# Performance work log

Measured on AMD Instinct MI355X. Metric: run time of the kernel, lower is better.

## Reference

```python
import jax, jax.numpy as jnp
import numpy as np

B, IN, H, O, L, G = 4096, 512, 1024, 256, 2, 3


def _lin_init(key, out_dim, in_dim):
    k1, k2 = jax.random.split(key)
    bound = 1.0 / np.sqrt(in_dim)
    w = jax.random.uniform(k1, (out_dim, in_dim), jnp.float32, -bound, bound)
    b = jax.random.uniform(k2, (out_dim,), jnp.float32, -bound, bound)
    return w, b


def setup_inputs() -> dict:
    key = jax.random.key(0)
    ks = jax.random.split(key, 10)
    x = jax.random.normal(ks[0], (B, IN), jnp.float32)
    hidden = jax.random.normal(ks[1], (L, B, H), jnp.float32)
    i2d_w, i2d_b = _lin_init(ks[2], H, IN)
    # stacked GRU params, PyTorch gate order (r, z, n); layer0 input dim == H (after i2d)
    kih = jax.random.split(ks[3], L)
    khh = jax.random.split(ks[4], L)
    gru_w_ih = jnp.stack([_lin_init(kih[l], 3 * H, H)[0] for l in range(L)])
    gru_b_ih = jnp.stack([_lin_init(kih[l], 3 * H, H)[1] for l in range(L)])
    gru_w_hh = jnp.stack([_lin_init(khh[l], 3 * H, H)[0] for l in range(L)])
    gru_b_hh = jnp.stack([_lin_init(khh[l], 3 * H, H)[1] for l in range(L)])
    mu_w, mu_b = _lin_init(ks[5], O * G, H)
    sigma_w, sigma_b = _lin_init(ks[6], O * G, H)
    pi_w, pi_b = _lin_init(ks[7], O * G, H)
    return {"x": x, "hidden": hidden, "i2d_w": i2d_w, "i2d_b": i2d_b,
            "gru_w_ih": gru_w_ih, "gru_w_hh": gru_w_hh,
            "gru_b_ih": gru_b_ih, "gru_b_hh": gru_b_hh,
            "mu_w": mu_w, "mu_b": mu_b, "sigma_w": sigma_w, "sigma_b": sigma_b,
            "pi_w": pi_w, "pi_b": pi_b, "batch_size": B}


def reference(x, hidden, i2d_w, i2d_b, gru_w_ih, gru_w_hh, gru_b_ih, gru_b_hh,
              mu_w, mu_b, sigma_w, sigma_b, pi_w, pi_b, batch_size):
    # input projection + relu
    h1 = jax.nn.relu(x @ i2d_w.T + i2d_b)  # [B, H]
    # single-timestep stacked GRU (PyTorch cell math, gate order r,z,n)
    inp = h1
    new_h = []
    for l in range(hidden.shape[0]):
        h_prev = hidden[l]
        gi = inp @ gru_w_ih[l].T + gru_b_ih[l]   # [B, 3H]
        gh = h_prev @ gru_w_hh[l].T + gru_b_hh[l]
        i_r, i_z, i_n = jnp.split(gi, 3, axis=-1)
        h_r, h_z, h_n = jnp.split(gh, 3, axis=-1)
        r = jax.nn.sigmoid(i_r + h_r)
        z = jax.nn.sigmoid(i_z + h_z)
        n = jnp.tanh(i_n + r * h_n)
        h_new = (1.0 - z) * n + z * h_prev
        new_h.append(h_new)
        inp = h_new
    hidden_out = jnp.stack(new_h)            # [L, B, H]
    h_out = jnp.tanh(inp)                    # [B, H]
    n_g = 3
    o = mu_w.shape[0] // n_g
    pi = jax.nn.softmax((h_out @ pi_w.T + pi_b).reshape(-1, n_g, o), axis=1)
    mu = (h_out @ mu_w.T + mu_b).reshape(-1, n_g, o)
    sig = jax.nn.softplus(h_out @ sigma_w.T + sigma_b).reshape(-1, n_g, o)
    return (mu, sig, pi, hidden_out)
```

## Files before the change

kernel.cpp:

```cpp
#include <hip/hip_runtime.h>
#include <stdint.h>

typedef unsigned short bf16u;
typedef float f32x4 __attribute__((ext_vector_type(4)));
typedef short bf16x8 __attribute__((ext_vector_type(8)));
typedef float f4 __attribute__((ext_vector_type(4)));

#define BM 128
#define BN 128
#define BK 64

__device__ __forceinline__ float b2f(bf16u u) {
  union { uint32_t i; float f; } v; v.i = ((uint32_t)u) << 16; return v.f;
}
__device__ __forceinline__ uint32_t f2b(float f) {
  union { float f; uint32_t i; } v; v.f = f;
  uint32_t i = v.i;
  return (i + 0x7FFFu + ((i >> 16) & 1u)) >> 16;
}
__device__ __forceinline__ float sigm(float x) { return 1.f / (1.f + __expf(-x)); }

__global__ __launch_bounds__(256)
void cvt_f32_bf16(const float* __restrict__ src, bf16u* __restrict__ dst) {
  size_t i = ((size_t)blockIdx.x * 256 + threadIdx.x) * 8;
  f4 a = *(const f4*)&src[i];
  f4 b = *(const f4*)&src[i + 4];
  uint4 o;
  o.x = (f2b(a[0]) & 0xffffu) | (f2b(a[1]) << 16);
  o.y = (f2b(a[2]) & 0xffffu) | (f2b(a[3]) << 16);
  o.z = (f2b(b[0]) & 0xffffu) | (f2b(b[1]) << 16);
  o.w = (f2b(b[2]) & 0xffffu) | (f2b(b[3]) << 16);
  *(uint4*)&dst[i] = o;
}

struct GemmPtrs {
  const bf16u* A[3];
  const bf16u* W[3];
  const float* bias[3];
  void* C[3];
};

template <int ACT, int OUTF32>
__global__ __launch_bounds__(256)
void gemm_bt(GemmPtrs p, int N, int K) {
  __shared__ bf16u sA[BM * BK];
  __shared__ bf16u sB[BN * BK];
  const int z = blockIdx.z;
  const bf16u* __restrict__ A = p.A[z];
  const bf16u* __restrict__ W = p.W[z];
  const float* __restrict__ bias = p.bias[z];

  const int tid  = threadIdx.x;
  const int wave = tid >> 6;
  const int lane = tid & 63;
  const int bn = blockIdx.x, bm = blockIdx.y;

  const int srow = wave * 32 + (lane >> 3);
  const int kc   = (lane & 7) ^ ((lane >> 3) & 7);
  const bf16u* ag = A + (size_t)(bm * BM + srow) * K + kc * 8;
  const bf16u* wg = W + (size_t)(bn * BN + srow) * K + kc * 8;

  const int wm = wave >> 1, wn = wave & 1;
  const int q = lane >> 4, cl = lane & 15;

  int aoff[4][2], boff[4][2];
#pragma unroll
  for (int i = 0; i < 4; ++i) {
    int m = wm * 64 + i * 16 + cl;
    int n = wn * 64 + i * 16 + cl;
#pragma unroll
    for (int kk = 0; kk < 2; ++kk) {
      aoff[i][kk] = m * 64 + (((q + kk * 4) ^ (m & 7)) * 8);
      boff[i][kk] = n * 64 + (((q + kk * 4) ^ (n & 7)) * 8);
    }
  }

  f32x4 acc[4][4] = {};

  for (int k0 = 0; k0 < K; k0 += BK) {
#pragma unroll
    for (int t = 0; t < 4; ++t) {
      __builtin_amdgcn_global_load_lds(
          (const __attribute__((address_space(1))) void*)(ag + k0 + (size_t)t * 8 * K),
          (__attribute__((address_space(3))) void*)&sA[wave * 2048 + t * 512],
          16, 0, 0);
      __builtin_amdgcn_global_load_lds(
          (const __attribute__((address_space(1))) void*)(wg + k0 + (size_t)t * 8 * K),
          (__attribute__((address_space(3))) void*)&sB[wave * 2048 + t * 512],
          16, 0, 0);
    }
    __syncthreads();
#pragma unroll
    for (int kk = 0; kk < 2; ++kk) {
      bf16x8 af[4], bfr[4];
#pragma unroll
      for (int i = 0; i < 4; ++i) af[i] = *(const bf16x8*)&sA[aoff[i][kk]];
#pragma unroll
      for (int j = 0; j < 4; ++j) bfr[j] = *(const bf16x8*)&sB[boff[j][kk]];
#pragma unroll
      for (int i = 0; i < 4; ++i)
#pragma unroll
        for (int j = 0; j < 4; ++j)
          acc[i][j] = __builtin_amdgcn_mfma_f32_16x16x32_bf16(af[i], bfr[j], acc[i][j], 0, 0, 0);
    }
    __syncthreads();
  }

  float bv[4];
#pragma unroll
  for (int j = 0; j < 4; ++j)
    bv[j] = bias[bn * BN + wn * 64 + j * 16 + cl];

  const int row0 = bm * BM + wm * 64 + q * 4;
  const int col0 = bn * BN + wn * 64 + cl;
#pragma unroll
  for (int i = 0; i < 4; ++i)
#pragma unroll
    for (int j = 0; j < 4; ++j)
#pragma unroll
      for (int r = 0; r < 4; ++r) {
        float v = acc[i][j][r] + bv[j];
        if (ACT == 1) v = fmaxf(v, 0.f);
        size_t off = (size_t)(row0 + i * 16 + r) * N + (col0 + j * 16);
        if (OUTF32) ((float*)p.C[z])[off] = v;
        else        ((bf16u*)p.C[z])[off] = (bf16u)f2b(v);
      }
}

struct __align__(16) V8 { uint32_t u[4]; };
__device__ __forceinline__ float getf(const V8& v, int k) {
  uint32_t w = v.u[k >> 1];
  return b2f((bf16u)((k & 1) ? (w >> 16) : (w & 0xffffu)));
}
__device__ __forceinline__ void setb(V8& v, int k, float f) {
  uint32_t b = f2b(f) & 0xffffu;
  if (k & 1) v.u[k >> 1] = (v.u[k >> 1] & 0x0000ffffu) | (b << 16);
  else       v.u[k >> 1] = (v.u[k >> 1] & 0xffff0000u) | b;
}

template <int LAST>
__global__ __launch_bounds__(256)
void gru_gates(const bf16u* __restrict__ gi, const bf16u* __restrict__ gh,
               const float* __restrict__ hprev, float* __restrict__ hid_out,
               bf16u* __restrict__ nxt) {
  int t = blockIdx.x * 256 + threadIdx.x;
  size_t idx = (size_t)t * 8;
  int b = (int)(idx >> 10);
  int h = (int)(idx & 1023);
  size_t g0 = (size_t)b * 3072 + h;
  V8 ir  = *(const V8*)&gi[g0];
  V8 izv = *(const V8*)&gi[g0 + 1024];
  V8 inv = *(const V8*)&gi[g0 + 2048];
  V8 hr  = *(const V8*)&gh[g0];
  V8 hzv = *(const V8*)&gh[g0 + 1024];
  V8 hnv = *(const V8*)&gh[g0 + 2048];
  f4 hp0 = *(const f4*)&hprev[idx];
  f4 hp1 = *(const f4*)&hprev[idx + 4];
  f4 o0, o1;
  V8 no = {};
#pragma unroll
  for (int k = 0; k < 8; ++k) {
    float hpv = (k < 4) ? hp0[k] : hp1[k - 4];
    float r  = sigm(getf(ir, k) + getf(hr, k));
    float zg = sigm(getf(izv, k) + getf(hzv, k));
    float n  = tanhf(getf(inv, k) + r * getf(hnv, k));
    float hnew = (1.f - zg) * n + zg * hpv;
    if (k < 4) o0[k] = hnew; else o1[k - 4] = hnew;
    setb(no, k, LAST ? tanhf(hnew) : hnew);
  }
  *(f4*)&hid_out[idx] = o0;
  *(f4*)&hid_out[idx + 4] = o1;
  *(V8*)&nxt[idx] = no;
}

__global__ __launch_bounds__(256)
void heads_ep(const float* __restrict__ raw, float* __restrict__ out,
              int rawHS, int outHS) {
  int t = blockIdx.x * 256 + threadIdx.x;
  int b = t >> 6;
  int o4 = (t & 63) << 2;
  size_t rb = (size_t)b * 768 + o4;
  f4 mu[3], sg[3], pi[3];
#pragma unroll
  for (int g = 0; g < 3; ++g) {
    mu[g] = *(const f4*)&raw[rb + g * 256];
    sg[g] = *(const f4*)&raw[(size_t)rawHS + rb + g * 256];
    pi[g] = *(const f4*)&raw[2 * (size_t)rawHS + rb + g * 256];
  }
  f4 pe[3];
#pragma unroll
  for (int c = 0; c < 4; ++c) {
    float m = fmaxf(fmaxf(pi[0][c], pi[1][c]), pi[2][c]);
    float e0 = __expf(pi[0][c] - m), e1 = __expf(pi[1][c] - m), e2 = __expf(pi[2][c] - m);
    float s = 1.f / (e0 + e1 + e2);
    pe[0][c] = e0 * s; pe[1][c] = e1 * s; pe[2][c] = e2 * s;
  }
#pragma unroll
  for (int g = 0; g < 3; ++g) {
    f4 sp;
#pragma unroll
    for (int c = 0; c < 4; ++c)
      sp[c] = fmaxf(sg[g][c], 0.f) + log1pf(__expf(-fabsf(sg[g][c])));
    *(f4*)&out[rb + g * 256]                     = mu[g];
    *(f4*)&out[(size_t)outHS + rb + g * 256]     = sp;
    *(f4*)&out[2 * (size_t)outHS + rb + g * 256] = pe[g];
  }
}

extern "C" void kernel_launch(void* const* d_in, const int* in_sizes, int n_in,
                              void* d_out, int out_size, void* d_ws, size_t ws_size,
                              hipStream_t stream) {
  const float* x      = (const float*)d_in[0];
  const float* hidden = (const float*)d_in[1];
  const float* i2d_w  = (const float*)d_in[2];
  const float* i2d_b  = (const float*)d_in[3];
  const float* w_ih   = (const float*)d_in[4];
  const float* w_hh   = (const float*)d_in[5];
  const float* b_ih   = (const float*)d_in[6];
  const float* b_hh   = (const float*)d_in[7];
  const float* mu_w   = (const float*)d_in[8];
  const float* mu_b   = (const float*)d_in[9];
  const float* sg_w   = (const float*)d_in[10];
  const float* sg_b   = (const float*)d_in[11];
  const float* pi_w   = (const float*)d_in[12];
  const float* pi_b   = (const float*)d_in[13];
  float* out = (float*)d_out;

  const size_t BH = 4194304;
  const int HS = 3145728;
  float* hid_base = out + (size_t)3 * HS;

  dim3 blk(256, 1, 1);

  bf16u* wb = (bf16u*)d_ws;
  bf16u* wb_i2d = wb;
  bf16u* wb_ih  = wb_i2d + 524288;
  bf16u* wb_hh  = wb_ih + 6291456;
  bf16u* wb_mu  = wb_hh + 6291456;
  bf16u* wb_sg  = wb_mu + 786432;
  bf16u* wb_pi  = wb_sg + 786432;
  const size_t wbytes = 30932992;

  cvt_f32_bf16<<<dim3(524288 / 2048), blk, 0, stream>>>(i2d_w, wb_i2d);
  cvt_f32_bf16<<<dim3(6291456 / 2048), blk, 0, stream>>>(w_ih, wb_ih);
  cvt_f32_bf16<<<dim3(6291456 / 2048), blk, 0, stream>>>(w_hh, wb_hh);
  cvt_f32_bf16<<<dim3(786432 / 2048), blk, 0, stream>>>(mu_w, wb_mu);
  cvt_f32_bf16<<<dim3(786432 / 2048), blk, 0, stream>>>(sg_w, wb_sg);
  cvt_f32_bf16<<<dim3(786432 / 2048), blk, 0, stream>>>(pi_w, wb_pi);

  int Bc = 4096;
  while (wbytes + (size_t)Bc * 19456 > ws_size && Bc > 256) Bc >>= 1;
  const int nchunk = 4096 / Bc;

  char* cbase = (char*)d_ws + wbytes;
  bf16u* ws0 = (bf16u*)cbase;
  bf16u* xb  = (bf16u*)(cbase + (size_t)Bc * 2048);
  bf16u* hb0 = (bf16u*)(cbase + (size_t)Bc * 3072);
  bf16u* hb1 = (bf16u*)(cbase + (size_t)Bc * 5120);
  bf16u* gi  = (bf16u*)(cbase + (size_t)Bc * 7168);
  bf16u* gh  = (bf16u*)(cbase + (size_t)Bc * 13312);
  float* raw = (float*)gi;
  const int rawHS = Bc * 768;
  const int gy = Bc / 128;

  for (int c = 0; c < nchunk; ++c) {
    const size_t off = (size_t)c * Bc;
    const float* h0_c = hidden + off * 1024;
    const float* h1_c = hidden + BH + off * 1024;

    cvt_f32_bf16<<<dim3(Bc * 512 / 2048), blk, 0, stream>>>(x + off * 512, xb);
    cvt_f32_bf16<<<dim3(Bc * 1024 / 2048), blk, 0, stream>>>(h0_c, hb0);
    cvt_f32_bf16<<<dim3(Bc * 1024 / 2048), blk, 0, stream>>>(h1_c, hb1);

    {
      GemmPtrs p{};
      p.A[0] = xb; p.W[0] = wb_i2d; p.bias[0] = i2d_b; p.C[0] = ws0;
      gemm_bt<1, 0><<<dim3(8, gy, 1), blk, 0, stream>>>(p, 1024, 512);
    }
    {
      GemmPtrs p{};
      p.A[0] = ws0; p.W[0] = wb_ih; p.bias[0] = b_ih; p.C[0] = gi;
      p.A[1] = hb0; p.W[1] = wb_hh; p.bias[1] = b_hh; p.C[1] = gh;
      gemm_bt<0, 0><<<dim3(24, gy, 2), blk, 0, stream>>>(p, 3072, 1024);
    }
    gru_gates<0><<<dim3(Bc / 2), blk, 0, stream>>>(
        gi, gh, h0_c, hid_base + off * 1024, ws0);
    {
      GemmPtrs p{};
      p.A[0] = ws0; p.W[0] = wb_ih + 3145728; p.bias[0] = b_ih + 3072; p.C[0] = gi;
      p.A[1] = hb1; p.W[1] = wb_hh + 3145728; p.bias[1] = b_hh + 3072; p.C[1] = gh;
      gemm_bt<0, 0><<<dim3(24, gy, 2), blk, 0, stream>>>(p, 3072, 1024);
    }
    gru_gates<1><<<dim3(Bc / 2), blk, 0, stream>>>(
        gi, gh, h1_c, hid_base + BH + off * 1024, ws0);
    {
      GemmPtrs p{};
      p.A[0] = ws0; p.W[0] = wb_mu; p.bias[0] = mu_b; p.C[0] = raw;
      p.A[1] = ws0; p.W[1] = wb_sg; p.bias[1] = sg_b; p.C[1] = raw + rawHS;
      p.A[2] = ws0; p.W[2] = wb_pi; p.bias[2] = pi_b; p.C[2] = raw + 2 * (size_t)rawHS;
      gemm_bt<0, 1><<<dim3(6, gy, 3), blk, 0, stream>>>(p, 768, 1024);
    }
    heads_ep<<<dim3(Bc / 4), blk, 0, stream>>>(raw, out + off * 768, rawHS, HS);
  }
}
```

Before: 402.8 us.

## Batch conversions into one launch, fuse head epilogues into GEMM, shrink small-GEMM tiles

Replaces the separate f32-to-bf16 conversion launches with a single multi-segment conversion kernel for the weights and another for the per-chunk activations. The three head GEMMs are merged into one launch over a concatenated weight matrix, and mu and softplus(sigma) are written straight to the output from the GEMM epilogue, so only the pi softmax remains as a separate pass. The GEMM M-tile becomes a template parameter, and the i2d and head GEMMs use 64-row tiles to launch more blocks. The intent is to cut launch overhead and the extra round trip of raw head outputs through memory, at the cost of per-element head branches in the epilogue and a segment search in the conversion kernel.

```diff
diff --git a/kernel.cpp b/kernel.cpp
--- a/kernel.cpp
+++ b/kernel.cpp
@@ -6,10 +6,6 @@
 typedef short bf16x8 __attribute__((ext_vector_type(8)));
 typedef float f4 __attribute__((ext_vector_type(4)));
 
-#define BM 128
-#define BN 128
-#define BK 64
-
 __device__ __forceinline__ float b2f(bf16u u) {
   union { uint32_t i; float f; } v; v.i = ((uint32_t)u) << 16; return v.f;
 }
@@ -20,31 +16,44 @@
 }
 __device__ __forceinline__ float sigm(float x) { return 1.f / (1.f + __expf(-x)); }
 
+struct CvtSeg { const float* src; char* dst; int blk0; int count; int tobf16; };
+struct CvtArgs { CvtSeg s[12]; int nseg; };
+
 __global__ __launch_bounds__(256)
-void cvt_f32_bf16(const float* __restrict__ src, bf16u* __restrict__ dst) {
-  size_t i = ((size_t)blockIdx.x * 256 + threadIdx.x) * 8;
-  f4 a = *(const f4*)&src[i];
-  f4 b = *(const f4*)&src[i + 4];
-  uint4 o;
-  o.x = (f2b(a[0]) & 0xffffu) | (f2b(a[1]) << 16);
-  o.y = (f2b(a[2]) & 0xffffu) | (f2b(a[3]) << 16);
-  o.z = (f2b(b[0]) & 0xffffu) | (f2b(b[1]) << 16);
-  o.w = (f2b(b[2]) & 0xffffu) | (f2b(b[3]) << 16);
-  *(uint4*)&dst[i] = o;
+void cvt_multi(CvtArgs a) {
+  int b = blockIdx.x, seg = 0;
+  while (seg + 1 < a.nseg && b >= a.s[seg + 1].blk0) ++seg;
+  const CvtSeg& S = a.s[seg];
+  size_t idx = ((size_t)(b - S.blk0) * 2048) + (size_t)threadIdx.x * 8;
+  if ((long long)idx >= S.count) return;
+  f4 x = *(const f4*)&S.src[idx];
+  f4 y = *(const f4*)&S.src[idx + 4];
+  if (S.tobf16) {
+    uint4 o;
+    o.x = (f2b(x[0]) & 0xffffu) | (f2b(x[1]) << 16);
+    o.y = (f2b(x[2]) & 0xffffu) | (f2b(x[3]) << 16);
+    o.z = (f2b(y[0]) & 0xffffu) | (f2b(y[1]) << 16);
+    o.w = (f2b(y[2]) & 0xffffu) | (f2b(y[3]) << 16);
+    *(uint4*)((bf16u*)S.dst + idx) = o;
+  } else {
+    *(f4*)((float*)S.dst + idx) = x;
+    *(f4*)((float*)S.dst + idx + 4) = y;
+  }
 }
 
 struct GemmPtrs {
-  const bf16u* A[3];
-  const bf16u* W[3];
-  const float* bias[3];
-  void* C[3];
+  const bf16u* A[2];
+  const bf16u* W[2];
+  const float* bias[2];
+  void* C[2];
 };
 
-template <int ACT, int OUTF32>
+template <int IT, int ACT, int OUTF32>
 __global__ __launch_bounds__(256)
 void gemm_bt(GemmPtrs p, int N, int K) {
-  __shared__ bf16u sA[BM * BK];
-  __shared__ bf16u sB[BN * BK];
+  constexpr int BM = IT * 32;
+  __shared__ bf16u sA[BM * 64];
+  __shared__ bf16u sB[128 * 64];
   const int z = blockIdx.z;
   const bf16u* __restrict__ A = p.A[z];
   const bf16u* __restrict__ W = p.W[z];
@@ -55,50 +64,56 @@
   const int lane = tid & 63;
   const int bn = blockIdx.x, bm = blockIdx.y;
 
-  const int srow = wave * 32 + (lane >> 3);
-  const int kc   = (lane & 7) ^ ((lane >> 3) & 7);
-  const bf16u* ag = A + (size_t)(bm * BM + srow) * K + kc * 8;
-  const bf16u* wg = W + (size_t)(bn * BN + srow) * K + kc * 8;
+  const int srA = wave * (IT * 8) + (lane >> 3);
+  const int srB = wave * 32 + (lane >> 3);
+  const int kc  = (lane & 7) ^ ((lane >> 3) & 7);
+  const bf16u* ag = A + (size_t)(bm * BM + srA) * K + kc * 8;
+  const bf16u* wg = W + (size_t)(bn * 128 + srB) * K + kc * 8;
 
   const int wm = wave >> 1, wn = wave & 1;
   const int q = lane >> 4, cl = lane & 15;
 
-  int aoff[4][2], boff[4][2];
-#pragma unroll
-  for (int i = 0; i < 4; ++i) {
-    int m = wm * 64 + i * 16 + cl;
-    int n = wn * 64 + i * 16 + cl;
-#pragma unroll
-    for (int kk = 0; kk < 2; ++kk) {
+  int aoff[IT][2], boff[4][2];
+#pragma unroll
+  for (int i = 0; i < IT; ++i) {
+    int m = wm * (IT * 16) + i * 16 + cl;
+#pragma unroll
+    for (int kk = 0; kk < 2; ++kk)
       aoff[i][kk] = m * 64 + (((q + kk * 4) ^ (m & 7)) * 8);
-      boff[i][kk] = n * 64 + (((q + kk * 4) ^ (n & 7)) * 8);
-    }
-  }
-
-  f32x4 acc[4][4] = {};
-
-  for (int k0 = 0; k0 < K; k0 += BK) {
-#pragma unroll
-    for (int t = 0; t < 4; ++t) {
+  }
+#pragma unroll
+  for (int j = 0; j < 4; ++j) {
+    int n = wn * 64 + j * 16 + cl;
+#pragma unroll
+    for (int kk = 0; kk < 2; ++kk)
+      boff[j][kk] = n * 64 + (((q + kk * 4) ^ (n & 7)) * 8);
+  }
+
+  f32x4 acc[IT][4] = {};
+
+  for (int k0 = 0; k0 < K; k0 += 64) {
+#pragma unroll
+    for (int t = 0; t < IT; ++t)
       __builtin_amdgcn_global_load_lds(
           (const __attribute__((address_space(1))) void*)(ag + k0 + (size_t)t * 8 * K),
-          (__attribute__((address_space(3))) void*)&sA[wave * 2048 + t * 512],
+          (__attribute__((address_space(3))) void*)&sA[wave * IT * 512 + t * 512],
           16, 0, 0);
+#pragma unroll
+    for (int t = 0; t < 4; ++t)
       __builtin_amdgcn_global_load_lds(
           (const __attribute__((address_space(1))) void*)(wg + k0 + (size_t)t * 8 * K),
           (__attribute__((address_space(3))) void*)&sB[wave * 2048 + t * 512],
           16, 0, 0);
-    }
     __syncthreads();
 #pragma unroll
     for (int kk = 0; kk < 2; ++kk) {
-      bf16x8 af[4], bfr[4];
-#pragma unroll
-      for (int i = 0; i < 4; ++i) af[i] = *(const bf16x8*)&sA[aoff[i][kk]];
+      bf16x8 af[IT], bfr[4];
+#pragma unroll
+      for (int i = 0; i < IT; ++i) af[i] = *(const bf16x8*)&sA[aoff[i][kk]];
 #pragma unroll
       for (int j = 0; j < 4; ++j) bfr[j] = *(const bf16x8*)&sB[boff[j][kk]];
 #pragma unroll
-      for (int i = 0; i < 4; ++i)
+      for (int i = 0; i < IT; ++i)
 #pragma unroll
         for (int j = 0; j < 4; ++j)
           acc[i][j] = __builtin_amdgcn_mfma_f32_16x16x32_bf16(af[i], bfr[j], acc[i][j], 0, 0, 0);
@@ -109,12 +124,12 @@
   float bv[4];
 #pragma unroll
   for (int j = 0; j < 4; ++j)
-    bv[j] = bias[bn * BN + wn * 64 + j * 16 + cl];
-
-  const int row0 = bm * BM + wm * 64 + q * 4;
-  const int col0 = bn * BN + wn * 64 + cl;
-#pragma unroll
-  for (int i = 0; i < 4; ++i)
+    bv[j] = bias[bn * 128 + wn * 64 + j * 16 + cl];
+
+  const int row0 = bm * BM + wm * (IT * 16) + q * 4;
+  const int col0 = bn * 128 + wn * 64 + cl;
+#pragma unroll
+  for (int i = 0; i < IT; ++i)
 #pragma unroll
     for (int j = 0; j < 4; ++j)
 #pragma unroll
@@ -124,6 +139,98 @@
         size_t off = (size_t)(row0 + i * 16 + r) * N + (col0 + j * 16);
         if (OUTF32) ((float*)p.C[z])[off] = v;
         else        ((bf16u*)p.C[z])[off] = (bf16u)f2b(v);
+      }
+}
+
+__global__ __launch_bounds__(256)
+void gemm_heads(const bf16u* __restrict__ A, const bf16u* __restrict__ Wp,
+                const float* __restrict__ biasp, float* __restrict__ out_mu,
+                float* __restrict__ out_sg, float* __restrict__ rawpi,
+                int outHS) {
+  constexpr int K = 1024;
+  __shared__ bf16u sA[64 * 64];
+  __shared__ bf16u sB[128 * 64];
+  const int tid  = threadIdx.x;
+  const int wave = tid >> 6;
+  const int lane = tid & 63;
+  const int bn = blockIdx.x, bm = blockIdx.y;
+
+  const int srA = wave * 16 + (lane >> 3);
+  const int srB = wave * 32 + (lane >> 3);
+  const int kc  = (lane & 7) ^ ((lane >> 3) & 7);
+  const bf16u* ag = A + (size_t)(bm * 64 + srA) * K + kc * 8;
+  const bf16u* wg = Wp + (size_t)(bn * 128 + srB) * K + kc * 8;
+
+  const int wm = wave >> 1, wn = wave & 1;
+  const int q = lane >> 4, cl = lane & 15;
+
+  int aoff[2][2], boff[4][2];
+#pragma unroll
+  for (int i = 0; i < 2; ++i) {
+    int m = wm * 32 + i * 16 + cl;
+#pragma unroll
+    for (int kk = 0; kk < 2; ++kk)
+      aoff[i][kk] = m * 64 + (((q + kk * 4) ^ (m & 7)) * 8);
+  }
+#pragma unroll
+  for (int j = 0; j < 4; ++j) {
+    int n = wn * 64 + j * 16 + cl;
+#pragma unroll
+    for (int kk = 0; kk < 2; ++kk)
+      boff[j][kk] = n * 64 + (((q + kk * 4) ^ (n & 7)) * 8);
+  }
+
+  f32x4 acc[2][4] = {};
+  for (int k0 = 0; k0 < K; k0 += 64) {
+#pragma unroll
+    for (int t = 0; t < 2; ++t)
+      __builtin_amdgcn_global_load_lds(
+          (const __attribute__((address_space(1))) void*)(ag + k0 + (size_t)t * 8 * K),
+          (__attribute__((address_space(3))) void*)&sA[wave * 1024 + t * 512],
+          16, 0, 0);
+#pragma unroll
+    for (int t = 0; t < 4; ++t)
+      __builtin_amdgcn_global_load_lds(
+          (const __attribute__((address_space(1))) void*)(wg + k0 + (size_t)t * 8 * K),
+          (__attribute__((address_space(3))) void*)&sB[wave * 2048 + t * 512],
+          16, 0, 0);
+    __syncthreads();
+#pragma unroll
+    for (int kk = 0; kk < 2; ++kk) {
+      bf16x8 af[2], bfr[4];
+#pragma unroll
+      for (int i = 0; i < 2; ++i) af[i] = *(const bf16x8*)&sA[aoff[i][kk]];
+#pragma unroll
+      for (int j = 0; j < 4; ++j) bfr[j] = *(const bf16x8*)&sB[boff[j][kk]];
+#pragma unroll
+      for (int i = 0; i < 2; ++i)
+#pragma unroll
+        for (int j = 0; j < 4; ++j)
+          acc[i][j] = __builtin_amdgcn_mfma_f32_16x16x32_bf16(af[i], bfr[j], acc[i][j], 0, 0, 0);
+    }
+    __syncthreads();
+  }
+
+  float bv[4];
+#pragma unroll
+  for (int j = 0; j < 4; ++j)
+    bv[j] = biasp[bn * 128 + wn * 64 + j * 16 + cl];
+
+  const int head = bn / 6;
+  const int ch0 = (bn % 6) * 128 + wn * 64 + cl;
+  const int row0 = bm * 64 + wm * 32 + q * 4;
+#pragma unroll
+  for (int i = 0; i < 2; ++i)
+#pragma unroll
+    for (int j = 0; j < 4; ++j)
+#pragma unroll
+      for (int r = 0; r < 4; ++r) {
+        float v = acc[i][j][r] + bv[j];
+        size_t off = (size_t)(row0 + i * 16 + r) * 768 + (ch0 + j * 16);
+        if (head == 0) out_mu[off] = v;
+        else if (head == 1)
+          out_sg[(size_t)0 + off] = fmaxf(v, 0.f) + log1pf(__expf(-fabsf(v)));
+        else rawpi[off] = v;
       }
 }
 
@@ -174,37 +281,25 @@
 }
 
 __global__ __launch_bounds__(256)
-void heads_ep(const float* __restrict__ raw, float* __restrict__ out,
-              int rawHS, int outHS) {
+void pi_softmax(const float* __restrict__ rawpi, float* __restrict__ out) {
   int t = blockIdx.x * 256 + threadIdx.x;
   int b = t >> 6;
   int o4 = (t & 63) << 2;
   size_t rb = (size_t)b * 768 + o4;
-  f4 mu[3], sg[3], pi[3];
-#pragma unroll
-  for (int g = 0; g < 3; ++g) {
-    mu[g] = *(const f4*)&raw[rb + g * 256];
-    sg[g] = *(const f4*)&raw[(size_t)rawHS + rb + g * 256];
-    pi[g] = *(const f4*)&raw[2 * (size_t)rawHS + rb + g * 256];
-  }
-  f4 pe[3];
+  f4 pi0 = *(const f4*)&rawpi[rb];
+  f4 pi1 = *(const f4*)&rawpi[rb + 256];
+  f4 pi2 = *(const f4*)&rawpi[rb + 512];
+  f4 e0v, e1v, e2v;
 #pragma unroll
   for (int c = 0; c < 4; ++c) {
-    float m = fmaxf(fmaxf(pi[0][c], pi[1][c]), pi[2][c]);
-    float e0 = __expf(pi[0][c] - m), e1 = __expf(pi[1][c] - m), e2 = __expf(pi[2][c] - m);
+    float m = fmaxf(fmaxf(pi0[c], pi1[c]), pi2[c]);
+    float e0 = __expf(pi0[c] - m), e1 = __expf(pi1[c] - m), e2 = __expf(pi2[c] - m);
     float s = 1.f / (e0 + e1 + e2);
-    pe[0][c] = e0 * s; pe[1][c] = e1 * s; pe[2][c] = e2 * s;
-  }
-#pragma unroll
-  for (int g = 0; g < 3; ++g) {
-    f4 sp;
-#pragma unroll
-    for (int c = 0; c < 4; ++c)
-      sp[c] = fmaxf(sg[g][c], 0.f) + log1pf(__expf(-fabsf(sg[g][c])));
-    *(f4*)&out[rb + g * 256]                     = mu[g];
-    *(f4*)&out[(size_t)outHS + rb + g * 256]     = sp;
-    *(f4*)&out[2 * (size_t)outHS + rb + g * 256] = pe[g];
-  }
+    e0v[c] = e0 * s; e1v[c] = e1 * s; e2v[c] = e2 * s;
+  }
+  *(f4*)&out[rb]       = e0v;
+  *(f4*)&out[rb + 256] = e1v;
+  *(f4*)&out[rb + 512] = e2v;
 }
 
 extern "C" void kernel_launch(void* const* d_in, const int* in_sizes, int n_in,
@@ -232,21 +327,31 @@
 
   dim3 blk(256, 1, 1);
 
-  bf16u* wb = (bf16u*)d_ws;
-  bf16u* wb_i2d = wb;
+  bf16u* wb_i2d = (bf16u*)d_ws;
   bf16u* wb_ih  = wb_i2d + 524288;
   bf16u* wb_hh  = wb_ih + 6291456;
-  bf16u* wb_mu  = wb_hh + 6291456;
-  bf16u* wb_sg  = wb_mu + 786432;
-  bf16u* wb_pi  = wb_sg + 786432;
-  const size_t wbytes = 30932992;
-
-  cvt_f32_bf16<<<dim3(524288 / 2048), blk, 0, stream>>>(i2d_w, wb_i2d);
-  cvt_f32_bf16<<<dim3(6291456 / 2048), blk, 0, stream>>>(w_ih, wb_ih);
-  cvt_f32_bf16<<<dim3(6291456 / 2048), blk, 0, stream>>>(w_hh, wb_hh);
-  cvt_f32_bf16<<<dim3(786432 / 2048), blk, 0, stream>>>(mu_w, wb_mu);
-  cvt_f32_bf16<<<dim3(786432 / 2048), blk, 0, stream>>>(sg_w, wb_sg);
-  cvt_f32_bf16<<<dim3(786432 / 2048), blk, 0, stream>>>(pi_w, wb_pi);
+  bf16u* wb_hd  = wb_hh + 6291456;
+  float* biasp  = (float*)((char*)d_ws + 30932992);
+  const size_t wbytes = 30942208;
+
+  {
+    CvtArgs a{};
+    int nb = 0;
+    auto seg = [&](const float* s, void* d, int count, int tobf) {
+      a.s[a.nseg++] = {s, (char*)d, nb, count, tobf};
+      nb += (count + 2047) / 2048;
+    };
+    seg(i2d_w, wb_i2d, 524288, 1);
+    seg(w_ih,  wb_ih, 6291456, 1);
+    seg(w_hh,  wb_hh, 6291456, 1);
+    seg(mu_w,  wb_hd, 786432, 1);
+    seg(sg_w,  wb_hd + 786432, 786432, 1);
+    seg(pi_w,  wb_hd + 1572864, 786432, 1);
+    seg(mu_b,  biasp, 768, 0);
+    seg(sg_b,  biasp + 768, 768, 0);
+    seg(pi_b,  biasp + 1536, 768, 0);
+    cvt_multi<<<dim3(nb), blk, 0, stream>>>(a);
+  }
 
   int Bc = 4096;
   while (wbytes + (size_t)Bc * 19456 > ws_size && Bc > 256) Bc >>= 1;
@@ -259,29 +364,36 @@
   bf16u* hb1 = (bf16u*)(cbase + (size_t)Bc * 5120);
   bf16u* gi  = (bf16u*)(cbase + (size_t)Bc * 7168);
   bf16u* gh  = (bf16u*)(cbase + (size_t)Bc * 13312);
-  float* raw = (float*)gi;
-  const int rawHS = Bc * 768;
-  const int gy = Bc / 128;
+  float* rawpi = (float*)gi;
 
   for (int c = 0; c < nchunk; ++c) {
     const size_t off = (size_t)c * Bc;
     const float* h0_c = hidden + off * 1024;
     const float* h1_c = hidden + BH + off * 1024;
 
-    cvt_f32_bf16<<<dim3(Bc * 512 / 2048), blk, 0, stream>>>(x + off * 512, xb);
-    cvt_f32_bf16<<<dim3(Bc * 1024 / 2048), blk, 0, stream>>>(h0_c, hb0);
-    cvt_f32_bf16<<<dim3(Bc * 1024 / 2048), blk, 0, stream>>>(h1_c, hb1);
+    {
+      CvtArgs a{};
+      int nb = 0;
+      auto seg = [&](const float* s, void* d, int count) {
+        a.s[a.nseg++] = {s, (char*)d, nb, count, 1};
+        nb += (count + 2047) / 2048;
+      };
+      seg(x + off * 512, xb, Bc * 512);
+      seg(h0_c, hb0, Bc * 1024);
+      seg(h1_c, hb1, Bc * 1024);
+      cvt_multi<<<dim3(nb), blk, 0, stream>>>(a);
+    }
 
     {
       GemmPtrs p{};
       p.A[0] = xb; p.W[0] = wb_i2d; p.bias[0] = i2d_b; p.C[0] = ws0;
-      gemm_bt<1, 0><<<dim3(8, gy, 1), blk, 0, stream>>>(p, 1024, 512);
+      gemm_bt<2, 1, 0><<<dim3(8, Bc / 64, 1), blk, 0, stream>>>(p, 1024, 512);
     }
     {
       GemmPtrs p{};
       p.A[0] = ws0; p.W[0] = wb_ih; p.bias[0] = b_ih; p.C[0] = gi;
       p.A[1] = hb0; p.W[1] = wb_hh; p.bias[1] = b_hh; p.C[1] = gh;
-      gemm_bt<0, 0><<<dim3(24, gy, 2), blk, 0, stream>>>(p, 3072, 1024);
+      gemm_bt<4, 0, 0><<<dim3(24, Bc / 128, 2), blk, 0, stream>>>(p, 3072, 1024);
     }
     gru_gates<0><<<dim3(Bc / 2), blk, 0, stream>>>(
         gi, gh, h0_c, hid_base + off * 1024, ws0);
@@ -289,17 +401,12 @@
       GemmPtrs p{};
       p.A[0] = ws0; p.W[0] = wb_ih + 3145728; p.bias[0] = b_ih + 3072; p.C[0] = gi;
       p.A[1] = hb1; p.W[1] = wb_hh + 3145728; p.bias[1] = b_hh + 3072; p.C[1] = gh;
-      gemm_bt<0, 0><<<dim3(24, gy, 2), blk, 0, stream>>>(p, 3072, 1024);
+      gemm_bt<4, 0, 0><<<dim3(24, Bc / 128, 2), blk, 0, stream>>>(p, 3072, 1024);
     }
     gru_gates<1><<<dim3(Bc / 2), blk, 0, stream>>>(
         gi, gh, h1_c, hid_base + BH + off * 1024, ws0);
-    {
-      GemmPtrs p{};
-      p.A[0] = ws0; p.W[0] = wb_mu; p.bias[0] = mu_b; p.C[0] = raw;
-      p.A[1] = ws0; p.W[1] = wb_sg; p.bias[1] = sg_b; p.C[1] = raw + rawHS;
-      p.A[2] = ws0; p.W[2] = wb_pi; p.bias[2] = pi_b; p.C[2] = raw + 2 * (size_t)rawHS;
-      gemm_bt<0, 1><<<dim3(6, gy, 3), blk, 0, stream>>>(p, 768, 1024);
-    }
-    heads_ep<<<dim3(Bc / 4), blk, 0, stream>>>(raw, out + off * 768, rawHS, HS);
-  }
-}
+    gemm_heads<<<dim3(18, Bc / 64, 1), blk, 0, stream>>>(
+        ws0, wb_hd, biasp, out + off * 768, out + HS + off * 768, rawpi, HS);
+    pi_softmax<<<dim3(Bc / 4), blk, 0, stream>>>(rawpi, out + 2 * (size_t)HS + off * 768);
+  }
+}
```

New measurement: 395.7 us. Within noise of the previous version (-1.8%).
